# Performance work log

Measured on AMD Instinct MI355X. Metric: run time of the kernel, lower is better.

## Reference

```python
import jax, jax.numpy as jnp
import numpy as np
import math

N_A = 100000
N_B = 100000
E = 400000
D = 128      # in_dim == out_dim (skip connection requires equality)
H = 8        # n_heads
DK = 16      # d_k = D // H
SQRT_DK = math.sqrt(DK)


def setup_inputs():
    ks = list(jax.random.split(jax.random.key(0), 32))
    it = iter(ks)

    def nrm(shape, s):
        return (jax.random.normal(next(it), shape) * s).astype(jnp.float32)

    def idx(n):
        return jax.random.randint(next(it), (E,), 0, n)

    inp = {}
    inp['x_a'] = nrm((N_A, D), 1.0)
    inp['x_b'] = nrm((N_B, D), 1.0)
    inp['src_ab'], inp['dst_ab'] = idx(N_A), idx(N_B)
    inp['src_ba'], inp['dst_ba'] = idx(N_B), idx(N_A)
    inp['src_bb'], inp['dst_bb'] = idx(N_B), idx(N_B)
    w_scale = math.sqrt(2.0 / (D + D))  # xavier-ish
    for t in ('a', 'b'):
        for m in ('k', 'q', 'v', 'a'):
            inp['W%s_%s' % (m, t)] = nrm((D, D), w_scale)
            inp['b%s_%s' % (m, t)] = jnp.zeros((D,), jnp.float32)
        inp['skip_%s' % t] = jnp.ones((1,), jnp.float32)
    r_scale = math.sqrt(2.0 / (DK + DK))
    for e in ('ab', 'ba', 'bb'):
        inp['pri_%s' % e] = jnp.ones((H,), jnp.float32)
        inp['att_%s' % e] = nrm((H, DK, DK), r_scale)
        inp['msg_%s' % e] = nrm((H, DK, DK), r_scale)
    return inp


def _etype_agg(k_src, q_dst, v_src, src, dst, att_w, msg_w, pri, n_dst):
    # gather src/dst node features onto edges: [E, H, DK]
    ke = k_src[src]
    # bmm(k.transpose(1,0), relation_att).transpose(1,0) == einsum ehd,hdf->ehf
    key_e = jnp.einsum('ehd,hdf->ehf', ke, att_w)
    a = jnp.sum(q_dst[dst] * key_e, axis=-1) * pri / SQRT_DK   # [E, H]
    val = jnp.einsum('ehd,hdf->ehf', v_src[src], msg_w)         # [E, H, DK]
    # ragged per-dst-node softmax over incoming edges (DGL mailbox softmax)
    amax = jax.ops.segment_max(a, dst, num_segments=n_dst)
    amax = jax.lax.stop_gradient(jnp.where(jnp.isfinite(amax), amax, 0.0))
    ea = jnp.exp(a - amax[dst])
    denom = jax.ops.segment_sum(ea, dst, num_segments=n_dst)
    w = ea / jnp.maximum(denom[dst], 1e-9)
    h = jax.ops.segment_sum(w[:, :, None] * val, dst, num_segments=n_dst)
    return jax.nn.relu(h.reshape(n_dst, H * DK))


def reference(x_a, x_b, src_ab, dst_ab, src_ba, dst_ba, src_bb, dst_bb,
              Wk_a, bk_a, Wq_a, bq_a, Wv_a, bv_a, Wa_a, ba_a, skip_a,
              Wk_b, bk_b, Wq_b, bq_b, Wv_b, bv_b, Wa_b, ba_b, skip_b,
              pri_ab, att_ab, msg_ab, pri_ba, att_ba, msg_ba,
              pri_bb, att_bb, msg_bb):
    n_a, n_b = x_a.shape[0], x_b.shape[0]
    k_a = (x_a @ Wk_a + bk_a).reshape(n_a, H, DK)
    q_a = (x_a @ Wq_a + bq_a).reshape(n_a, H, DK)
    v_a = (x_a @ Wv_a + bv_a).reshape(n_a, H, DK)
    k_b = (x_b @ Wk_b + bk_b).reshape(n_b, H, DK)
    q_b = (x_b @ Wq_b + bq_b).reshape(n_b, H, DK)
    v_b = (x_b @ Wv_b + bv_b).reshape(n_b, H, DK)

    # per-etype attention + softmax + weighted aggregate
    t_b1 = _etype_agg(k_a, q_b, v_a, src_ab, dst_ab, att_ab, msg_ab, pri_ab, n_b)
    t_b2 = _etype_agg(k_b, q_b, v_b, src_bb, dst_bb, att_bb, msg_bb, pri_bb, n_b)
    t_b = 0.5 * (t_b1 + t_b2)        # cross_reducer='mean' over {ab, bb}
    t_a = _etype_agg(k_b, q_a, v_b, src_ba, dst_ba, att_ba, msg_ba, pri_ba, n_a)

    alpha_a = jax.nn.sigmoid(skip_a)
    out_a = (t_a @ Wa_a + ba_a) * alpha_a + x_a * (1.0 - alpha_a)
    alpha_b = jax.nn.sigmoid(skip_b)
    out_b = (t_b @ Wa_b + ba_b) * alpha_b + x_b * (1.0 - alpha_b)
    # dropout is identity in eval; use_norm=False
    return jnp.stack([out_a, out_b])  # [2, N, D]
```

## Files before the change

kernel.cpp:

```cpp
#include <hip/hip_runtime.h>
#include <hip/hip_bf16.h>
#include <stdint.h>

#define D 128
#define H 8
#define DK 16

#define SCAN_BLK 256
#define SCAN_ITEMS 8
#define SCAN_TILE (SCAN_BLK * SCAN_ITEMS)
#define NBUCK 192

typedef __attribute__((ext_vector_type(8))) short bf16x8;
typedef __attribute__((ext_vector_type(4))) float f32x4;

__device__ __forceinline__ unsigned short f2bf(float f) {
    unsigned int u = __float_as_uint(f);
    u = u + 0x7fffu + ((u >> 16) & 1u);
    return (unsigned short)(u >> 16);
}
__device__ __forceinline__ float bfl(unsigned int u) { return __uint_as_float(u << 16); }
__device__ __forceinline__ float bfh(unsigned int u) { return __uint_as_float(u & 0xffff0000u); }
__device__ __forceinline__ unsigned int pack2(unsigned short a, unsigned short b) {
    return (unsigned int)a | ((unsigned int)b << 16);
}
__device__ __forceinline__ void unpack8(uint4 u, float* o) {
    o[0]=bfl(u.x); o[1]=bfh(u.x); o[2]=bfl(u.y); o[3]=bfh(u.y);
    o[4]=bfl(u.z); o[5]=bfh(u.z); o[6]=bfl(u.w); o[7]=bfh(u.w);
}

struct WTIn  { const float* w[4]; };
struct WTOut { unsigned short* wt[4]; };
struct FoldArgs {
    const float* W[6]; const float* R[6]; const float* b[6];
    unsigned short* WT[6]; float* bf[6]; int mode[6];
};

__global__ __launch_bounds__(256) void prep_kernel(WTIn in, WTOut out, FoldArgs a,
                                                   int* __restrict__ cnt, int S,
                                                   int nz, int* __restrict__ dhd) {
    __shared__ float tile[32][33];
    __shared__ float Wl[128 * 17];
    __shared__ float Rl[256];
    int bid = blockIdx.x;
    int tid = threadIdx.x;
    if (bid < 64) {
        int mat = bid >> 4;
        int t = bid & 15;
        int k0 = (t >> 2) * 32, c0 = (t & 3) * 32;
        const float* W = in.w[mat];
        unsigned short* WT = out.wt[mat];
        int lr = tid >> 5, lc = tid & 31;
        #pragma unroll
        for (int p = 0; p < 4; ++p)
            tile[p * 8 + lr][lc] = W[(size_t)(k0 + p * 8 + lr) * D + c0 + lc];
        __syncthreads();
        #pragma unroll
        for (int p = 0; p < 4; ++p)
            WT[(size_t)(c0 + p * 8 + lr) * D + k0 + lc] = f2bf(tile[lc][p * 8 + lr]);
    } else if (bid < 112) {
        int v = (bid - 64) >> 3, h = (bid - 64) & 7;
        const float* W = a.W[v];
        #pragma unroll
        for (int p = 0; p < 8; ++p) {
            int idx = p * 256 + tid;
            int c = idx >> 4, i = idx & 15;
            Wl[c * 17 + i] = W[(size_t)c * D + h * 16 + i];
        }
        Rl[tid] = a.R[v][h * 256 + tid];
        __syncthreads();
        int mode = a.mode[v];
        int c = tid & 127, jb = (tid >> 7) * 8;
        #pragma unroll
        for (int jj = 0; jj < 8; ++jj) {
            int j = jb + jj;
            float s = 0.f;
            #pragma unroll
            for (int i = 0; i < 16; ++i)
                s = fmaf(Wl[c * 17 + i], mode ? Rl[i * 16 + j] : Rl[j * 16 + i], s);
            a.WT[v][(size_t)(h * 16 + j) * D + c] = f2bf(s);
        }
        if (tid < 16) {
            const float* b = a.b[v];
            float s = 0.f;
            #pragma unroll
            for (int i = 0; i < 16; ++i)
                s = fmaf(b[h * 16 + i], mode ? Rl[i * 16 + tid] : Rl[tid * 16 + i], s);
            a.bf[v][h * 16 + tid] = s;
        }
    } else if (bid < 112 + nz) {
        int base = (bid - 112) * 1024 + tid * 4;
        if (base + 4 <= S) {
            *(int4*)&cnt[base] = make_int4(0, 0, 0, 0);
        } else {
            for (int i = base; i < S; ++i) cnt[i] = 0;
        }
    } else {
        for (int i = tid; i < 2 * NBUCK; i += 256) dhd[i] = 0;
    }
}

#define ASTRIDE 136
struct ProjFusedArgs {
    const float* X[2];
    int N[2], nmat[2], nblk0;
    const unsigned short* wt[2][5];
    const float* bias[2][5];
    unsigned short* out[2][5];
};

__global__ __launch_bounds__(256) void proj_fused_kernel(ProjFusedArgs a)
{
    __shared__ unsigned short As[64 * ASTRIDE];
    __shared__ unsigned short Cs[64 * ASTRIDE];
    const int tid = threadIdx.x;
    const int w = tid >> 6;
    const int l = tid & 63;
    const int seg = (blockIdx.x >= a.nblk0) ? 1 : 0;
    const int row0 = (blockIdx.x - (seg ? a.nblk0 : 0)) * 64;
    const float* X = a.X[seg];
    const int N = a.N[seg];
    const int nm = a.nmat[seg];

    #pragma unroll
    for (int p = 0; p < 8; ++p) {
        int f = p * 256 + tid;
        int r = f >> 5;
        int c4 = f & 31;
        int row = row0 + r; if (row >= N) row = N - 1;
        float4 xv = *(const float4*)&X[(size_t)row * D + c4 * 4];
        unsigned int lo = pack2(f2bf(xv.x), f2bf(xv.y));
        unsigned int hi = pack2(f2bf(xv.z), f2bf(xv.w));
        *(uint2*)&As[r * ASTRIDE + c4 * 4] = make_uint2(lo, hi);
    }
    __syncthreads();

    const int lrow = l & 15;
    const int lk8 = (l >> 4) * 8;

    for (int m = 0; m < nm; ++m) {
        const unsigned short* WT = a.wt[seg][m];
        bf16x8 bfrag[2][4];
        #pragma unroll
        for (int cf = 0; cf < 2; ++cf)
            #pragma unroll
            for (int kc = 0; kc < 4; ++kc)
                bfrag[cf][kc] = *(const bf16x8*)&WT[(size_t)(w * 32 + cf * 16 + lrow) * D + kc * 32 + lk8];

        f32x4 acc[4][2];
        #pragma unroll
        for (int rf = 0; rf < 4; ++rf) {
            acc[rf][0] = (f32x4){0.f, 0.f, 0.f, 0.f};
            acc[rf][1] = (f32x4){0.f, 0.f, 0.f, 0.f};
        }
        #pragma unroll
        for (int rf = 0; rf < 4; ++rf) {
            bf16x8 afrag[4];
            #pragma unroll
            for (int kc = 0; kc < 4; ++kc)
                afrag[kc] = *(const bf16x8*)&As[(rf * 16 + lrow) * ASTRIDE + kc * 32 + lk8];
            #pragma unroll
            for (int kc = 0; kc < 4; ++kc) {
                acc[rf][0] = __builtin_amdgcn_mfma_f32_16x16x32_bf16(afrag[kc], bfrag[0][kc], acc[rf][0], 0, 0, 0);
                acc[rf][1] = __builtin_amdgcn_mfma_f32_16x16x32_bf16(afrag[kc], bfrag[1][kc], acc[rf][1], 0, 0, 0);
            }
        }
        float bias0 = a.bias[seg][m][w * 32 + lrow];
        float bias1 = a.bias[seg][m][w * 32 + 16 + lrow];
        #pragma unroll
        for (int rf = 0; rf < 4; ++rf) {
            #pragma unroll
            for (int r = 0; r < 4; ++r) {
                int lr = rf * 16 + (l >> 4) * 4 + r;
                Cs[lr * ASTRIDE + w * 32 + lrow]      = f2bf(acc[rf][0][r] + bias0);
                Cs[lr * ASTRIDE + w * 32 + 16 + lrow] = f2bf(acc[rf][1][r] + bias1);
            }
        }
        __syncthreads();
        unsigned short* O = a.out[seg][m];
        #pragma unroll
        for (int p = 0; p < 4; ++p) {
            int idx = p * 256 + tid;
            int r = idx >> 4, c8 = idx & 15;
            int row = row0 + r;
            if (row < N)
                *(uint4*)&O[(size_t)row * D + c8 * 8] = *(const uint4*)&Cs[r * ASTRIDE + c8 * 8];
        }
        __syncthreads();
    }
}

struct OutFusedArgs {
    const unsigned short* T1[2]; const unsigned short* T2[2];
    const unsigned short* WT[2]; const float* bias[2];
    const float* skip[2]; const float* X[2]; float* O[2];
    int N[2], nsrc[2], nblk0;
};

__global__ __launch_bounds__(256) void out_fused_kernel(OutFusedArgs a)
{
    __shared__ unsigned short As[64 * ASTRIDE];
    const int tid = threadIdx.x;
    const int w = tid >> 6;
    const int l = tid & 63;
    const int seg = (blockIdx.x >= a.nblk0) ? 1 : 0;
    const int row0 = (blockIdx.x - (seg ? a.nblk0 : 0)) * 64;
    const int N = a.N[seg];
    const int nsrc = a.nsrc[seg];
    const unsigned short* T1 = a.T1[seg];
    const unsigned short* T2 = a.T2[seg];

    #pragma unroll
    for (int p = 0; p < 4; ++p) {
        int idx = p * 256 + tid;
        int r = idx >> 4;
        int c8 = idx & 15;
        int row = row0 + r; if (row >= N) row = N - 1;
        uint4 tv = *(const uint4*)&T1[(size_t)row * D + c8 * 8];
        float v[8]; unpack8(tv, v);
        #pragma unroll
        for (int i = 0; i < 8; ++i) v[i] = fmaxf(v[i], 0.f);
        if (nsrc == 2) {
            uint4 uv = *(const uint4*)&T2[(size_t)row * D + c8 * 8];
            float u[8]; unpack8(uv, u);
            #pragma unroll
            for (int i = 0; i < 8; ++i) v[i] = 0.5f * (v[i] + fmaxf(u[i], 0.f));
        }
        uint4 pk;
        pk.x = pack2(f2bf(v[0]), f2bf(v[1]));
        pk.y = pack2(f2bf(v[2]), f2bf(v[3]));
        pk.z = pack2(f2bf(v[4]), f2bf(v[5]));
        pk.w = pack2(f2bf(v[6]), f2bf(v[7]));
        *(uint4*)&As[r * ASTRIDE + c8 * 8] = pk;
    }
    __syncthreads();

    const int lrow = l & 15;
    const int lk8 = (l >> 4) * 8;
    const unsigned short* WT = a.WT[seg];

    bf16x8 bfrag[2][4];
    #pragma unroll
    for (int cf = 0; cf < 2; ++cf)
        #pragma unroll
        for (int kc = 0; kc < 4; ++kc)
            bfrag[cf][kc] = *(const bf16x8*)&WT[(size_t)(w * 32 + cf * 16 + lrow) * D + kc * 32 + lk8];

    f32x4 acc[4][2];
    #pragma unroll
    for (int rf = 0; rf < 4; ++rf) {
        acc[rf][0] = (f32x4){0.f, 0.f, 0.f, 0.f};
        acc[rf][1] = (f32x4){0.f, 0.f, 0.f, 0.f};
    }
    #pragma unroll
    for (int rf = 0; rf < 4; ++rf) {
        bf16x8 afrag[4];
        #pragma unroll
        for (int kc = 0; kc < 4; ++kc)
            afrag[kc] = *(const bf16x8*)&As[(rf * 16 + lrow) * ASTRIDE + kc * 32 + lk8];
        #pragma unroll
        for (int kc = 0; kc < 4; ++kc) {
            acc[rf][0] = __builtin_amdgcn_mfma_f32_16x16x32_bf16(afrag[kc], bfrag[0][kc], acc[rf][0], 0, 0, 0);
            acc[rf][1] = __builtin_amdgcn_mfma_f32_16x16x32_bf16(afrag[kc], bfrag[1][kc], acc[rf][1], 0, 0, 0);
        }
    }
    float alpha = 1.f / (1.f + __expf(-a.skip[seg][0]));
    float om = 1.f - alpha;
    float bias0 = a.bias[seg][w * 32 + lrow];
    float bias1 = a.bias[seg][w * 32 + 16 + lrow];
    const float* X = a.X[seg];
    float* O = a.O[seg];
    #pragma unroll
    for (int rf = 0; rf < 4; ++rf) {
        #pragma unroll
        for (int r = 0; r < 4; ++r) {
            int row = row0 + rf * 16 + (l >> 4) * 4 + r;
            if (row < N) {
                int c0 = w * 32 + lrow;
                float x0 = X[(size_t)row * D + c0];
                float x1 = X[(size_t)row * D + c0 + 16];
                O[(size_t)row * D + c0]      = (acc[rf][0][r] + bias0) * alpha + x0 * om;
                O[(size_t)row * D + c0 + 16] = (acc[rf][1][r] + bias1) * alpha + x1 * om;
            }
        }
    }
}

struct EdgeArgs {
    const int* src[3]; const int* dst[3]; int base[3]; int E;
};

__global__ __launch_bounds__(256) void hist_all_kernel(EdgeArgs a, int* __restrict__ cnt) {
    int gid = blockIdx.x * 256 + threadIdx.x;
    int E = a.E;
    if (gid >= 3 * E) return;
    int t = (gid < E) ? 0 : ((gid < 2 * E) ? 1 : 2);
    int e = gid - t * E;
    atomicAdd(&cnt[a.base[t] + a.dst[t][e]], 1);
}

__global__ __launch_bounds__(SCAN_BLK) void scan1_kernel(
    const int* __restrict__ cnt, int* __restrict__ bsum,
    int* __restrict__ dhist, int n, int n_b)
{
    __shared__ int sh[SCAN_BLK];
    __shared__ int lh[NBUCK];
    int tid = threadIdx.x;
    if (tid < NBUCK) lh[tid] = 0;
    __syncthreads();
    int base = blockIdx.x * SCAN_TILE + tid * SCAN_ITEMS;
    int s = 0;
    #pragma unroll
    for (int i = 0; i < SCAN_ITEMS; ++i) {
        int idx = base + i;
        if (idx < n) {
            int d = cnt[idx];
            s += d;
            int t = (idx < n_b) ? 0 : ((idx < 2 * n_b) ? 1 : 2);
            int dc = d > 63 ? 63 : d;
            atomicAdd(&lh[t * 64 + 63 - dc], 1);
        }
    }
    sh[tid] = s; __syncthreads();
    for (int o = SCAN_BLK / 2; o > 0; o >>= 1) {
        if (tid < o) sh[tid] += sh[tid + o];
        __syncthreads();
    }
    if (tid == 0) bsum[blockIdx.x] = sh[0];
    if (tid < NBUCK && lh[tid]) atomicAdd(&dhist[tid], lh[tid]);
}

__global__ __launch_bounds__(SCAN_BLK) void scan3_kernel(
    const int* __restrict__ cnt, const int* __restrict__ bsum,
    int* __restrict__ offs, int* __restrict__ cursor, int n)
{
    __shared__ int red[SCAN_BLK];
    __shared__ int sh[SCAN_BLK];
    const int tid = threadIdx.x;
    int pre = 0;
    for (int i = tid; i < blockIdx.x; i += SCAN_BLK) pre += bsum[i];
    red[tid] = pre; __syncthreads();
    for (int o = SCAN_BLK / 2; o > 0; o >>= 1) {
        if (tid < o) red[tid] += red[tid + o];
        __syncthreads();
    }
    int base0 = red[0];

    int base = blockIdx.x * SCAN_TILE + tid * SCAN_ITEMS;
    int v[SCAN_ITEMS];
    int s = 0;
    #pragma unroll
    for (int i = 0; i < SCAN_ITEMS; ++i) {
        int idx = base + i;
        v[i] = (idx < n) ? cnt[idx] : 0;
        s += v[i];
    }
    sh[tid] = s; __syncthreads();
    for (int o = 1; o < SCAN_BLK; o <<= 1) {
        int t = (tid >= o) ? sh[tid - o] : 0;
        __syncthreads();
        sh[tid] += t;
        __syncthreads();
    }
    int off = base0 + sh[tid] - s;
    #pragma unroll
    for (int i = 0; i < SCAN_ITEMS; ++i) {
        int idx = base + i;
        if (idx < n) {
            offs[idx] = off;
            cursor[idx] = off;
            off += v[i];
            if (idx == n - 1) offs[n] = off;
        }
    }
}

__global__ __launch_bounds__(256) void scatter_all_kernel(
    EdgeArgs a, int* __restrict__ cursor, int* __restrict__ csr_src)
{
    int gid = blockIdx.x * 256 + threadIdx.x;
    int E = a.E;
    if (gid >= 3 * E) return;
    int t = (gid < E) ? 0 : ((gid < 2 * E) ? 1 : 2);
    int e = gid - t * E;
    int p = atomicAdd(&cursor[a.base[t] + a.dst[t][e]], 1);
    csr_src[p] = a.src[t][e];
}

__global__ __launch_bounds__(256) void deg_scatter_kernel(
    const int* __restrict__ cnt, const int* __restrict__ dhist, int* __restrict__ dcur,
    int* __restrict__ perm, int S, int n_b)
{
    __shared__ int sc[256];
    __shared__ int excl[NBUCK];
    __shared__ int lcnt[NBUCK];
    __shared__ int lbase[NBUCK];
    int tid = threadIdx.x;
    int v = (tid < NBUCK) ? dhist[tid] : 0;
    sc[tid] = v; __syncthreads();
    for (int o = 1; o < 256; o <<= 1) {
        int t = (tid >= o) ? sc[tid - o] : 0;
        __syncthreads();
        sc[tid] += t;
        __syncthreads();
    }
    if (tid < NBUCK) { excl[tid] = sc[tid] - v; lcnt[tid] = 0; }
    __syncthreads();
    int i = blockIdx.x * 256 + tid;
    bool valid = (i < S);
    int b = 0, r = 0;
    if (valid) {
        int t = (i < n_b) ? 0 : ((i < 2 * n_b) ? 1 : 2);
        int d = cnt[i]; if (d > 63) d = 63;
        b = t * 64 + 63 - d;
        r = atomicAdd(&lcnt[b], 1);
    }
    __syncthreads();
    if (tid < NBUCK && lcnt[tid]) lbase[tid] = excl[tid] + atomicAdd(&dcur[tid], lcnt[tid]);
    __syncthreads();
    if (valid) perm[lbase[b] + r] = i;
}

struct AggArgs {
    const unsigned short* K[3];
    const unsigned short* Q[3];
    const unsigned short* V[3];
    const float* pri[3];
    unsigned short* T[3];
};

__global__ __launch_bounds__(256) void csr_agg_all_kernel(
    const int* __restrict__ offs, const int* __restrict__ csr_src,
    const int* __restrict__ perm, AggArgs a, int n_b, int n_a)
{
    int gid = blockIdx.x * 256 + threadIdx.x;
    int si = gid >> 4;
    int hp = gid & 15;
    int h = hp >> 1, p = hp & 1;
    int S = 2 * n_b + n_a;
    if (si >= S) return;
    int s = perm[si];
    int t = (s < n_b) ? 0 : ((s < 2 * n_b) ? 1 : 2);
    int n = s - ((t == 2) ? 2 * n_b : t * n_b);

    const unsigned short *Kp, *Qp, *Vp; const float* prip; unsigned short* Tp;
    if (t == 0)      { Kp=a.K[0]; Qp=a.Q[0]; Vp=a.V[0]; prip=a.pri[0]; Tp=a.T[0]; }
    else if (t == 1) { Kp=a.K[1]; Qp=a.Q[1]; Vp=a.V[1]; prip=a.pri[1]; Tp=a.T[1]; }
    else             { Kp=a.K[2]; Qp=a.Q[2]; Vp=a.V[2]; prip=a.pri[2]; Tp=a.T[2]; }

    int e0 = offs[s], e1 = offs[s + 1];
    const int sub = h * DK + p * 8;

    uint4 q = *(const uint4*)(Qp + (size_t)n * D + sub);
    float qv[8]; unpack8(q, qv);
    float ps = prip[h] * 0.25f;

    float acc[8];
    #pragma unroll
    for (int i = 0; i < 8; ++i) acc[i] = 0.f;
    float den = 0.f;

    int e = e0;
    for (; e + 2 <= e1; e += 2) {
        int s0 = csr_src[e], s1 = csr_src[e + 1];
        uint4 k0 = *(const uint4*)(Kp + (size_t)s0 * D + sub);
        uint4 v0 = *(const uint4*)(Vp + (size_t)s0 * D + sub);
        uint4 k1 = *(const uint4*)(Kp + (size_t)s1 * D + sub);
        uint4 v1 = *(const uint4*)(Vp + (size_t)s1 * D + sub);
        float ka[8], kb[8];
        unpack8(k0, ka); unpack8(k1, kb);
        float d0 = 0.f, d1 = 0.f;
        #pragma unroll
        for (int i = 0; i < 8; ++i) {
            d0 = fmaf(ka[i], qv[i], d0);
            d1 = fmaf(kb[i], qv[i], d1);
        }
        d0 += __shfl_xor(d0, 1, 64);
        d1 += __shfl_xor(d1, 1, 64);
        float ea0 = __expf(d0 * ps);
        float ea1 = __expf(d1 * ps);
        den += ea0 + ea1;
        float va[8], vb[8];
        unpack8(v0, va); unpack8(v1, vb);
        #pragma unroll
        for (int i = 0; i < 8; ++i)
            acc[i] = fmaf(ea0, va[i], fmaf(ea1, vb[i], acc[i]));
    }
    if (e < e1) {
        int s0 = csr_src[e];
        uint4 k = *(const uint4*)(Kp + (size_t)s0 * D + sub);
        uint4 v = *(const uint4*)(Vp + (size_t)s0 * D + sub);
        float kv[8]; unpack8(k, kv);
        float d = 0.f;
        #pragma unroll
        for (int i = 0; i < 8; ++i) d = fmaf(kv[i], qv[i], d);
        d += __shfl_xor(d, 1, 64);
        float ea = __expf(d * ps);
        den += ea;
        float vv[8]; unpack8(v, vv);
        #pragma unroll
        for (int i = 0; i < 8; ++i) acc[i] = fmaf(ea, vv[i], acc[i]);
    }
    float inv = 1.f / fmaxf(den, 1e-9f);
    unsigned short ob[8];
    #pragma unroll
    for (int i = 0; i < 8; ++i) ob[i] = f2bf(acc[i] * inv);
    uint4 o0;
    o0.x = pack2(ob[0], ob[1]);  o0.y = pack2(ob[2], ob[3]);
    o0.z = pack2(ob[4], ob[5]);  o0.w = pack2(ob[6], ob[7]);
    *(uint4*)(Tp + (size_t)n * D + sub) = o0;
}

extern "C" void kernel_launch(void* const* d_in, const int* in_sizes, int n_in,
                              void* d_out, int out_size, void* d_ws, size_t ws_size,
                              hipStream_t stream) {
    const float* x_a = (const float*)d_in[0];
    const float* x_b = (const float*)d_in[1];
    const int* src_ab = (const int*)d_in[2];
    const int* dst_ab = (const int*)d_in[3];
    const int* src_ba = (const int*)d_in[4];
    const int* dst_ba = (const int*)d_in[5];
    const int* src_bb = (const int*)d_in[6];
    const int* dst_bb = (const int*)d_in[7];
    const float* Wk_a = (const float*)d_in[8];  const float* bk_a = (const float*)d_in[9];
    const float* Wq_a = (const float*)d_in[10]; const float* bq_a = (const float*)d_in[11];
    const float* Wv_a = (const float*)d_in[12]; const float* bv_a = (const float*)d_in[13];
    const float* Wa_a = (const float*)d_in[14]; const float* ba_a = (const float*)d_in[15];
    const float* skip_a = (const float*)d_in[16];
    const float* Wk_b = (const float*)d_in[17]; const float* bk_b = (const float*)d_in[18];
    const float* Wq_b = (const float*)d_in[19]; const float* bq_b = (const float*)d_in[20];
    const float* Wv_b = (const float*)d_in[21]; const float* bv_b = (const float*)d_in[22];
    const float* Wa_b = (const float*)d_in[23]; const float* ba_b = (const float*)d_in[24];
    const float* skip_b = (const float*)d_in[25];
    const float* pri_ab = (const float*)d_in[26];
    const float* att_ab = (const float*)d_in[27];
    const float* msg_ab = (const float*)d_in[28];
    const float* pri_ba = (const float*)d_in[29];
    const float* att_ba = (const float*)d_in[30];
    const float* msg_ba = (const float*)d_in[31];
    const float* pri_bb = (const float*)d_in[32];
    const float* att_bb = (const float*)d_in[33];
    const float* msg_bb = (const float*)d_in[34];

    const int n_a = in_sizes[0] / D;
    const int n_b = in_sizes[1] / D;
    const int E = in_sizes[2];
    const int S = 2 * n_b + n_a;

    size_t off = 0;
    char* base = (char*)d_ws;
    auto alloc = [&](size_t bytes) -> void* {
        void* r = base + off;
        off += (bytes + 255) & ~(size_t)255;
        return r;
    };
    unsigned short* k_a = (unsigned short*)alloc((size_t)n_a * D * 2);
    unsigned short* k_b = (unsigned short*)alloc((size_t)n_b * D * 2);
    unsigned short* qab = (unsigned short*)alloc((size_t)n_b * D * 2);
    unsigned short* qbb = (unsigned short*)alloc((size_t)n_b * D * 2);
    unsigned short* qba = (unsigned short*)alloc((size_t)n_a * D * 2);
    unsigned short* vab = (unsigned short*)alloc((size_t)n_a * D * 2);
    unsigned short* vbb = (unsigned short*)alloc((size_t)n_b * D * 2);
    unsigned short* vba = (unsigned short*)alloc((size_t)n_b * D * 2);
    unsigned short* t_a  = (unsigned short*)alloc((size_t)n_a * D * 2);
    unsigned short* t_b1 = (unsigned short*)alloc((size_t)n_b * D * 2);
    unsigned short* t_b2 = (unsigned short*)alloc((size_t)n_b * D * 2);
    int* cnt    = (int*)alloc((size_t)S * 4);
    int* offs   = (int*)alloc(((size_t)S + 1) * 4);
    int* cursor = (int*)alloc((size_t)S * 4);
    int* csr_src= (int*)alloc((size_t)3 * E * 4);
    int* bsum   = (int*)alloc(256 * 4);
    int* dhd    = (int*)alloc(2 * NBUCK * 4);
    int* dhist  = dhd;
    int* dcur   = dhd + NBUCK;
    int* perm   = (int*)alloc((size_t)S * 4);
    unsigned short* wt_plain[4];
    for (int i = 0; i < 4; ++i) wt_plain[i] = (unsigned short*)alloc((size_t)D * D * 2);
    unsigned short* wt_fold[6];
    float* bf_fold[6];
    for (int i = 0; i < 6; ++i) {
        wt_fold[i] = (unsigned short*)alloc((size_t)D * D * 2);
        bf_fold[i] = (float*)alloc((size_t)D * 4);
    }

    WTIn win; WTOut wout;
    const float* worig[4] = {Wk_a, Wk_b, Wa_a, Wa_b};
    for (int i = 0; i < 4; ++i) { win.w[i] = worig[i]; wout.wt[i] = wt_plain[i]; }
    FoldArgs fa;
    const float* fW[6] = {Wq_b, Wq_b, Wq_a, Wv_a, Wv_b, Wv_b};
    const float* fR[6] = {att_ab, att_bb, att_ba, msg_ab, msg_bb, msg_ba};
    const float* fb[6] = {bq_b, bq_b, bq_a, bv_a, bv_b, bv_b};
    int fm[6] = {0, 0, 0, 1, 1, 1};
    for (int i = 0; i < 6; ++i) {
        fa.W[i] = fW[i]; fa.R[i] = fR[i]; fa.b[i] = fb[i];
        fa.WT[i] = wt_fold[i]; fa.bf[i] = bf_fold[i]; fa.mode[i] = fm[i];
    }
    int nz = (S + 1023) / 1024;
    prep_kernel<<<112 + nz + 1, 256, 0, stream>>>(win, wout, fa, cnt, S, nz, dhd);

    EdgeArgs ea;
    ea.src[0] = src_ab; ea.dst[0] = dst_ab;
    ea.src[1] = src_bb; ea.dst[1] = dst_bb;
    ea.src[2] = src_ba; ea.dst[2] = dst_ba;
    ea.base[0] = 0; ea.base[1] = n_b; ea.base[2] = 2 * n_b;
    ea.E = E;
    int ge3 = (3 * E + 255) / 256;
    hist_all_kernel<<<ge3, 256, 0, stream>>>(ea, cnt);
    int nb = (S + SCAN_TILE - 1) / SCAN_TILE;
    scan1_kernel<<<nb, SCAN_BLK, 0, stream>>>(cnt, bsum, dhist, S, n_b);
    scan3_kernel<<<nb, SCAN_BLK, 0, stream>>>(cnt, bsum, offs, cursor, S);
    scatter_all_kernel<<<ge3, 256, 0, stream>>>(ea, cursor, csr_src);

    int gS = (S + 255) / 256;
    deg_scatter_kernel<<<gS, 256, 0, stream>>>(cnt, dhist, dcur, perm, S, n_b);

    const int gb_a = (n_a + 63) / 64;
    const int gb_b = (n_b + 63) / 64;
    ProjFusedArgs pa;
    pa.X[0] = x_a; pa.N[0] = n_a; pa.nmat[0] = 3;
    pa.X[1] = x_b; pa.N[1] = n_b; pa.nmat[1] = 5;
    pa.nblk0 = gb_a;
    pa.wt[0][0] = wt_plain[0]; pa.bias[0][0] = bk_a;       pa.out[0][0] = k_a;
    pa.wt[0][1] = wt_fold[2];  pa.bias[0][1] = bf_fold[2]; pa.out[0][1] = qba;
    pa.wt[0][2] = wt_fold[3];  pa.bias[0][2] = bf_fold[3]; pa.out[0][2] = vab;
    pa.wt[0][3] = wt_plain[0]; pa.bias[0][3] = bk_a;       pa.out[0][3] = k_a;
    pa.wt[0][4] = wt_plain[0]; pa.bias[0][4] = bk_a;       pa.out[0][4] = k_a;
    pa.wt[1][0] = wt_plain[1]; pa.bias[1][0] = bk_b;       pa.out[1][0] = k_b;
    pa.wt[1][1] = wt_fold[0];  pa.bias[1][1] = bf_fold[0]; pa.out[1][1] = qab;
    pa.wt[1][2] = wt_fold[1];  pa.bias[1][2] = bf_fold[1]; pa.out[1][2] = qbb;
    pa.wt[1][3] = wt_fold[4];  pa.bias[1][3] = bf_fold[4]; pa.out[1][3] = vbb;
    pa.wt[1][4] = wt_fold[5];  pa.bias[1][4] = bf_fold[5]; pa.out[1][4] = vba;
    proj_fused_kernel<<<gb_a + gb_b, 256, 0, stream>>>(pa);

    AggArgs aa;
    aa.K[0] = k_a; aa.Q[0] = qab; aa.V[0] = vab; aa.pri[0] = pri_ab; aa.T[0] = t_b1;
    aa.K[1] = k_b; aa.Q[1] = qbb; aa.V[1] = vbb; aa.pri[1] = pri_bb; aa.T[1] = t_b2;
    aa.K[2] = k_b; aa.Q[2] = qba; aa.V[2] = vba; aa.pri[2] = pri_ba; aa.T[2] = t_a;
    int gs = (S * 16 + 255) / 256;
    csr_agg_all_kernel<<<gs, 256, 0, stream>>>(offs, csr_src, perm, aa, n_b, n_a);

    float* out_a = (float*)d_out;
    float* out_b = (float*)d_out + (size_t)n_a * D;
    OutFusedArgs oa;
    oa.T1[0] = t_a;  oa.T2[0] = t_a;  oa.WT[0] = wt_plain[2]; oa.bias[0] = ba_a;
    oa.skip[0] = skip_a; oa.X[0] = x_a; oa.O[0] = out_a; oa.N[0] = n_a; oa.nsrc[0] = 1;
    oa.T1[1] = t_b1; oa.T2[1] = t_b2; oa.WT[1] = wt_plain[3]; oa.bias[1] = ba_b;
    oa.skip[1] = skip_b; oa.X[1] = x_b; oa.O[1] = out_b; oa.N[1] = n_b; oa.nsrc[1] = 2;
    oa.nblk0 = gb_a;
    out_fused_kernel<<<gb_a + gb_b, 256, 0, stream>>>(oa);
}
```

Baseline: 404.4 us.

## Record per-edge rank in histogram and drop degree-sorted node permutation

The histogram kernel now saves each edge's atomic return value as its rank, so the scatter step computes CSR positions as offs + rank without a second round of atomics or a cursor array. The degree-bucket sorting of destination nodes, its per-block histograms and the deg_scatter kernel are removed, and aggregation walks destination nodes in natural order. This removes one kernel launch and the atomic and extra pass work in CSR construction. The cost is a 3E rank buffer and the loss of degree-balanced scheduling, which may increase wavefront divergence in the aggregation kernel.

```diff
diff --git a/kernel.cpp b/kernel.cpp
--- a/kernel.cpp
+++ b/kernel.cpp
@@ -9,7 +9,6 @@
 #define SCAN_BLK 256
 #define SCAN_ITEMS 8
 #define SCAN_TILE (SCAN_BLK * SCAN_ITEMS)
-#define NBUCK 192
 
 typedef __attribute__((ext_vector_type(8))) short bf16x8;
 typedef __attribute__((ext_vector_type(4))) float f32x4;
@@ -37,8 +36,7 @@
 };
 
 __global__ __launch_bounds__(256) void prep_kernel(WTIn in, WTOut out, FoldArgs a,
-                                                   int* __restrict__ cnt, int S,
-                                                   int nz, int* __restrict__ dhd) {
+                                                   int* __restrict__ cnt, int S) {
     __shared__ float tile[32][33];
     __shared__ float Wl[128 * 17];
     __shared__ float Rl[256];
@@ -88,15 +86,13 @@
                 s = fmaf(b[h * 16 + i], mode ? Rl[i * 16 + tid] : Rl[tid * 16 + i], s);
             a.bf[v][h * 16 + tid] = s;
         }
-    } else if (bid < 112 + nz) {
+    } else {
         int base = (bid - 112) * 1024 + tid * 4;
         if (base + 4 <= S) {
             *(int4*)&cnt[base] = make_int4(0, 0, 0, 0);
         } else {
             for (int i = base; i < S; ++i) cnt[i] = 0;
         }
-    } else {
-        for (int i = tid; i < 2 * NBUCK; i += 256) dhd[i] = 0;
     }
 }
 
@@ -290,36 +286,27 @@
     const int* src[3]; const int* dst[3]; int base[3]; int E;
 };
 
-__global__ __launch_bounds__(256) void hist_all_kernel(EdgeArgs a, int* __restrict__ cnt) {
+__global__ __launch_bounds__(256) void hist_all_kernel(EdgeArgs a, int* __restrict__ cnt,
+                                                       int* __restrict__ rank) {
     int gid = blockIdx.x * 256 + threadIdx.x;
     int E = a.E;
     if (gid >= 3 * E) return;
     int t = (gid < E) ? 0 : ((gid < 2 * E) ? 1 : 2);
     int e = gid - t * E;
-    atomicAdd(&cnt[a.base[t] + a.dst[t][e]], 1);
+    rank[gid] = atomicAdd(&cnt[a.base[t] + a.dst[t][e]], 1);
 }
 
 __global__ __launch_bounds__(SCAN_BLK) void scan1_kernel(
-    const int* __restrict__ cnt, int* __restrict__ bsum,
-    int* __restrict__ dhist, int n, int n_b)
+    const int* __restrict__ cnt, int* __restrict__ bsum, int n)
 {
     __shared__ int sh[SCAN_BLK];
-    __shared__ int lh[NBUCK];
     int tid = threadIdx.x;
-    if (tid < NBUCK) lh[tid] = 0;
-    __syncthreads();
     int base = blockIdx.x * SCAN_TILE + tid * SCAN_ITEMS;
     int s = 0;
     #pragma unroll
     for (int i = 0; i < SCAN_ITEMS; ++i) {
         int idx = base + i;
-        if (idx < n) {
-            int d = cnt[idx];
-            s += d;
-            int t = (idx < n_b) ? 0 : ((idx < 2 * n_b) ? 1 : 2);
-            int dc = d > 63 ? 63 : d;
-            atomicAdd(&lh[t * 64 + 63 - dc], 1);
-        }
+        if (idx < n) s += cnt[idx];
     }
     sh[tid] = s; __syncthreads();
     for (int o = SCAN_BLK / 2; o > 0; o >>= 1) {
@@ -327,12 +314,11 @@
         __syncthreads();
     }
     if (tid == 0) bsum[blockIdx.x] = sh[0];
-    if (tid < NBUCK && lh[tid]) atomicAdd(&dhist[tid], lh[tid]);
 }
 
 __global__ __launch_bounds__(SCAN_BLK) void scan3_kernel(
     const int* __restrict__ cnt, const int* __restrict__ bsum,
-    int* __restrict__ offs, int* __restrict__ cursor, int n)
+    int* __restrict__ offs, int n)
 {
     __shared__ int red[SCAN_BLK];
     __shared__ int sh[SCAN_BLK];
@@ -368,7 +354,6 @@
         int idx = base + i;
         if (idx < n) {
             offs[idx] = off;
-            cursor[idx] = off;
             off += v[i];
             if (idx == n - 1) offs[n] = off;
         }
@@ -376,49 +361,16 @@
 }
 
 __global__ __launch_bounds__(256) void scatter_all_kernel(
-    EdgeArgs a, int* __restrict__ cursor, int* __restrict__ csr_src)
+    EdgeArgs a, const int* __restrict__ offs, const int* __restrict__ rank,
+    int* __restrict__ csr_src)
 {
     int gid = blockIdx.x * 256 + threadIdx.x;
     int E = a.E;
     if (gid >= 3 * E) return;
     int t = (gid < E) ? 0 : ((gid < 2 * E) ? 1 : 2);
     int e = gid - t * E;
-    int p = atomicAdd(&cursor[a.base[t] + a.dst[t][e]], 1);
+    int p = offs[a.base[t] + a.dst[t][e]] + rank[gid];
     csr_src[p] = a.src[t][e];
-}
-
-__global__ __launch_bounds__(256) void deg_scatter_kernel(
-    const int* __restrict__ cnt, const int* __restrict__ dhist, int* __restrict__ dcur,
-    int* __restrict__ perm, int S, int n_b)
-{
-    __shared__ int sc[256];
-    __shared__ int excl[NBUCK];
-    __shared__ int lcnt[NBUCK];
-    __shared__ int lbase[NBUCK];
-    int tid = threadIdx.x;
-    int v = (tid < NBUCK) ? dhist[tid] : 0;
-    sc[tid] = v; __syncthreads();
-    for (int o = 1; o < 256; o <<= 1) {
-        int t = (tid >= o) ? sc[tid - o] : 0;
-        __syncthreads();
-        sc[tid] += t;
-        __syncthreads();
-    }
-    if (tid < NBUCK) { excl[tid] = sc[tid] - v; lcnt[tid] = 0; }
-    __syncthreads();
-    int i = blockIdx.x * 256 + tid;
-    bool valid = (i < S);
-    int b = 0, r = 0;
-    if (valid) {
-        int t = (i < n_b) ? 0 : ((i < 2 * n_b) ? 1 : 2);
-        int d = cnt[i]; if (d > 63) d = 63;
-        b = t * 64 + 63 - d;
-        r = atomicAdd(&lcnt[b], 1);
-    }
-    __syncthreads();
-    if (tid < NBUCK && lcnt[tid]) lbase[tid] = excl[tid] + atomicAdd(&dcur[tid], lcnt[tid]);
-    __syncthreads();
-    if (valid) perm[lbase[b] + r] = i;
 }
 
 struct AggArgs {
@@ -431,7 +383,7 @@
 
 __global__ __launch_bounds__(256) void csr_agg_all_kernel(
     const int* __restrict__ offs, const int* __restrict__ csr_src,
-    const int* __restrict__ perm, AggArgs a, int n_b, int n_a)
+    AggArgs a, int n_b, int n_a)
 {
     int gid = blockIdx.x * 256 + threadIdx.x;
     int si = gid >> 4;
@@ -439,7 +391,7 @@
     int h = hp >> 1, p = hp & 1;
     int S = 2 * n_b + n_a;
     if (si >= S) return;
-    int s = perm[si];
+    int s = si;
     int t = (s < n_b) ? 0 : ((s < 2 * n_b) ? 1 : 2);
     int n = s - ((t == 2) ? 2 * n_b : t * n_b);
 
@@ -567,13 +519,9 @@
     unsigned short* t_b2 = (unsigned short*)alloc((size_t)n_b * D * 2);
     int* cnt    = (int*)alloc((size_t)S * 4);
     int* offs   = (int*)alloc(((size_t)S + 1) * 4);
-    int* cursor = (int*)alloc((size_t)S * 4);
+    int* rank   = (int*)alloc((size_t)3 * E * 4);
     int* csr_src= (int*)alloc((size_t)3 * E * 4);
     int* bsum   = (int*)alloc(256 * 4);
-    int* dhd    = (int*)alloc(2 * NBUCK * 4);
-    int* dhist  = dhd;
-    int* dcur   = dhd + NBUCK;
-    int* perm   = (int*)alloc((size_t)S * 4);
     unsigned short* wt_plain[4];
     for (int i = 0; i < 4; ++i) wt_plain[i] = (unsigned short*)alloc((size_t)D * D * 2);
     unsigned short* wt_fold[6];
@@ -596,7 +544,7 @@
         fa.WT[i] = wt_fold[i]; fa.bf[i] = bf_fold[i]; fa.mode[i] = fm[i];
     }
     int nz = (S + 1023) / 1024;
-    prep_kernel<<<112 + nz + 1, 256, 0, stream>>>(win, wout, fa, cnt, S, nz, dhd);
+    prep_kernel<<<112 + nz, 256, 0, stream>>>(win, wout, fa, cnt, S);
 
     EdgeArgs ea;
     ea.src[0] = src_ab; ea.dst[0] = dst_ab;
@@ -605,14 +553,11 @@
     ea.base[0] = 0; ea.base[1] = n_b; ea.base[2] = 2 * n_b;
     ea.E = E;
     int ge3 = (3 * E + 255) / 256;
-    hist_all_kernel<<<ge3, 256, 0, stream>>>(ea, cnt);
+    hist_all_kernel<<<ge3, 256, 0, stream>>>(ea, cnt, rank);
     int nb = (S + SCAN_TILE - 1) / SCAN_TILE;
-    scan1_kernel<<<nb, SCAN_BLK, 0, stream>>>(cnt, bsum, dhist, S, n_b);
-    scan3_kernel<<<nb, SCAN_BLK, 0, stream>>>(cnt, bsum, offs, cursor, S);
-    scatter_all_kernel<<<ge3, 256, 0, stream>>>(ea, cursor, csr_src);
-
-    int gS = (S + 255) / 256;
-    deg_scatter_kernel<<<gS, 256, 0, stream>>>(cnt, dhist, dcur, perm, S, n_b);
+    scan1_kernel<<<nb, SCAN_BLK, 0, stream>>>(cnt, bsum, S);
+    scan3_kernel<<<nb, SCAN_BLK, 0, stream>>>(cnt, bsum, offs, S);
+    scatter_all_kernel<<<ge3, 256, 0, stream>>>(ea, offs, rank, csr_src);
 
     const int gb_a = (n_a + 63) / 64;
     const int gb_b = (n_b + 63) / 64;
@@ -637,7 +582,7 @@
     aa.K[1] = k_b; aa.Q[1] = qbb; aa.V[1] = vbb; aa.pri[1] = pri_bb; aa.T[1] = t_b2;
     aa.K[2] = k_b; aa.Q[2] = qba; aa.V[2] = vba; aa.pri[2] = pri_ba; aa.T[2] = t_a;
     int gs = (S * 16 + 255) / 256;
-    csr_agg_all_kernel<<<gs, 256, 0, stream>>>(offs, csr_src, perm, aa, n_b, n_a);
+    csr_agg_all_kernel<<<gs, 256, 0, stream>>>(offs, csr_src, aa, n_b, n_a);
 
     float* out_a = (float*)d_out;
     float* out_b = (float*)d_out + (size_t)n_a * D;
```

Measured after the change: 353.2 us. 1.15x faster.
